# Optimization experiments

Hardware: AMD Instinct MI355X
Metric: run time of the kernel (lower is better)

## Reference

```python
import jax, jax.numpy as jnp
import numpy as np

B, S, HD, HE = 32, 2048, 1024, 1024

def setup_inputs() -> dict:
    key = jax.random.key(0)
    k1, k2, k3, k4, k5, k6 = jax.random.split(key, 6)
    decoder_hidden = jax.random.normal(k1, (B, HD), dtype=jnp.float32)
    encoder_outputs = jax.random.normal(k2, (B, S, HE), dtype=jnp.float32)
    src_mask = jax.random.randint(k3, (B, S), 0, 2) > 0
    # nn.Linear weights stored as [out, in]; apply as x @ W.T
    s_q = 1.0 / np.sqrt(HD)
    s_k = 1.0 / np.sqrt(HE)
    W_query = jax.random.uniform(k4, (HD, HD), jnp.float32, -s_q, s_q)
    W_key = jax.random.uniform(k5, (HD, HE), jnp.float32, -s_k, s_k)
    W_energy = jax.random.uniform(k6, (1, HD), jnp.float32, -s_q, s_q)
    return {
        "decoder_hidden": decoder_hidden,
        "encoder_outputs": encoder_outputs,
        "src_mask": src_mask,
        "W_query": W_query,
        "W_key": W_key,
        "W_energy": W_energy,
    }

def reference(decoder_hidden, encoder_outputs, src_mask, W_query, W_key, W_energy):
    # q: [B, 1, HD], k: [B, S, HD]
    q = (decoder_hidden @ W_query.T)[:, None, :]
    k = jnp.einsum("bse,de->bsd", encoder_outputs, W_key)
    # scores: [B, S] = v^T tanh(q + k)
    scores = jnp.einsum("bsd,d->bs", jnp.tanh(q + k), W_energy[0])
    scores = jnp.where(src_mask, scores, -1e9)
    attn_weights = jax.nn.softmax(scores, axis=-1)
    context = jnp.einsum("bs,bse->be", attn_weights, encoder_outputs)
    return context, attn_weights
```

## Files before the change

kernel.cpp:

```cpp
#include <hip/hip_runtime.h>
#include <hip/hip_bf16.h>


#define NB 32
#define SS 2048
#define HD 1024
#define HE 1024
#define MM (NB * SS)
#define NT 32

typedef float f32x4 __attribute__((ext_vector_type(4)));
typedef short bf16x8 __attribute__((ext_vector_type(8)));
typedef short short4v __attribute__((ext_vector_type(4)));

static __device__ __forceinline__ short f2bf(float f) {
    union { __hip_bfloat16 h; short s; } u;
    u.h = __float2bfloat16(f);
    return u.s;
}
static __device__ __forceinline__ float bf2f(short s) {
    union { float f; unsigned u; } u;
    u.u = ((unsigned)(unsigned short)s) << 16;
    return u.f;
}

static __device__ __forceinline__ void gload16(const void* g, const void* l) {
    __builtin_amdgcn_global_load_lds(
        (const __attribute__((address_space(1))) void*)(uintptr_t)(g),
        (__attribute__((address_space(3))) void*)(unsigned)(uintptr_t)(l),
        16, 0, 0);
}

__global__ __launch_bounds__(64) void compact_kernel(const int* __restrict__ mask,
                                                     int* __restrict__ idx,
                                                     int* __restrict__ cnt) {
    const int b = blockIdx.x;
    const int lane = threadIdx.x;
    int base = 0;
    for (int s0 = 0; s0 < SS; s0 += 64) {
        const int m = mask[b * SS + s0 + lane];
        const unsigned long long bal = __ballot(m != 0);
        const int rank = __popcll(bal & ((1ull << lane) - 1ull));
        if (m) idx[b * SS + base + rank] = s0 + lane;
        base += (int)__popcll(bal);
    }
    if (lane == 0) cnt[b] = base;
    for (int j = base + lane; j < SS; j += 64) idx[b * SS + j] = 0;
}

__global__ __launch_bounds__(256) void zero_kernel(float* __restrict__ p, int n) {
    const int i = blockIdx.x * 256 + threadIdx.x;
    if (i < n) p[i] = 0.f;
}

__global__ __launch_bounds__(256) void cvt_bf16_kernel(const float* __restrict__ in,
                                                       short* __restrict__ out, int n8) {
    int i = blockIdx.x * 256 + threadIdx.x;
    const int stride = gridDim.x * 256;
    for (; i < n8; i += stride) {
        const f32x4 a = *(const f32x4*)(in + (long)i * 8);
        const f32x4 b = *(const f32x4*)(in + (long)i * 8 + 4);
        bf16x8 o;
        o[0] = f2bf(a[0]); o[1] = f2bf(a[1]); o[2] = f2bf(a[2]); o[3] = f2bf(a[3]);
        o[4] = f2bf(b[0]); o[5] = f2bf(b[1]); o[6] = f2bf(b[2]); o[7] = f2bf(b[3]);
        *(bf16x8*)(out + (long)i * 8) = o;
    }
}

__global__ __launch_bounds__(256) void cvt_enc_kernel(const float* __restrict__ enc,
                                                      const int* __restrict__ idx,
                                                      const int* __restrict__ cnt,
                                                      short* __restrict__ encb) {
    const int b  = blockIdx.x >> 7;
    const int j0 = (blockIdx.x & 127) * 16;
    const int n  = cnt[b];
    const int nr = (n + 127) & ~127;
    if (j0 >= nr) return;
    const int j  = j0 + (threadIdx.x >> 4);
    const int c0 = (threadIdx.x & 15) * 8;
    short* dst = encb + ((long)b * SS + j) * HE + c0;
    if (j < n) {
        const float* src = enc + ((long)b * SS + idx[b * SS + j]) * HE + c0;
        #pragma unroll
        for (int u = 0; u < 8; ++u) {
            const f32x4 x = *(const f32x4*)(src + u * 128);
            const f32x4 y = *(const f32x4*)(src + u * 128 + 4);
            bf16x8 o;
            o[0] = f2bf(x[0]); o[1] = f2bf(x[1]); o[2] = f2bf(x[2]); o[3] = f2bf(x[3]);
            o[4] = f2bf(y[0]); o[5] = f2bf(y[1]); o[6] = f2bf(y[2]); o[7] = f2bf(y[3]);
            *(bf16x8*)(dst + u * 128) = o;
        }
    } else {
        const bf16x8 z = (bf16x8){0,0,0,0,0,0,0,0};
        #pragma unroll
        for (int u = 0; u < 8; ++u) *(bf16x8*)(dst + u * 128) = z;
    }
}

__global__ __launch_bounds__(256) void qproj_kernel(const float* __restrict__ dh,
                                                    const float* __restrict__ Wq,
                                                    float* __restrict__ q) {
    const int wid  = threadIdx.x >> 6;
    const int lane = threadIdx.x & 63;
    const int d    = blockIdx.x * 4 + wid;
    const float* wrow = Wq + (long)d * HD + lane * 16;
    f32x4 w0 = *(const f32x4*)(wrow + 0);
    f32x4 w1 = *(const f32x4*)(wrow + 4);
    f32x4 w2 = *(const f32x4*)(wrow + 8);
    f32x4 w3 = *(const f32x4*)(wrow + 12);
    for (int b = 0; b < NB; ++b) {
        const float* drow = dh + b * HD + lane * 16;
        f32x4 d0 = *(const f32x4*)(drow + 0);
        f32x4 d1 = *(const f32x4*)(drow + 4);
        f32x4 d2 = *(const f32x4*)(drow + 8);
        f32x4 d3 = *(const f32x4*)(drow + 12);
        f32x4 s4 = w0 * d0 + w1 * d1 + w2 * d2 + w3 * d3;
        float dot = s4[0] + s4[1] + s4[2] + s4[3];
        #pragma unroll
        for (int off = 32; off > 0; off >>= 1)
            dot += __shfl_xor(dot, off, 64);
        if (lane == 0) q[b * HD + d] = dot;
    }
}

__global__ __launch_bounds__(256, 3) void score_mfma_kernel(const short* __restrict__ encb,
                                                            const short* __restrict__ wkb,
                                                            const float* __restrict__ qv,
                                                            const float* __restrict__ ven,
                                                            const int* __restrict__ cnt,
                                                            float* __restrict__ sp) {
    __shared__ __align__(16) short As[4096];
    __shared__ __align__(16) short Bs[4096];

    const int bid   = blockIdx.x;
    const int xcd   = bid & 7;
    const int slot  = bid >> 3;
    const int mtile = xcd * 64 + (slot >> 3);
    const int nt    = slot & 7;

    const int bb   = mtile >> 4;
    const int tile = mtile & 15;
    if (tile * 128 >= cnt[bb]) return;

    const int tid  = threadIdx.x;
    const int lane = tid & 63;
    const int wid  = tid >> 6;
    const int wr   = wid >> 1;
    const int wc   = wid & 1;
    const long mbase = (long)bb * SS + tile * 128;
    const int  nbase = nt * 128;

    f32x4 acc[4][4];
    #pragma unroll
    for (int m = 0; m < 4; ++m)
        #pragma unroll
        for (int n = 0; n < 4; ++n)
            acc[m][n] = (f32x4){0.f, 0.f, 0.f, 0.f};

    const short* ag0 = encb + (mbase + (tid >> 2)) * (long)HE + (tid & 3) * 8;
    const short* ag1 = ag0 + 64 * (long)HE;
    const short* bg0 = wkb + ((long)(nbase + (tid >> 2))) * HE + (tid & 3) * 8;
    const short* bg1 = bg0 + 64 * (long)HE;

    const int frow = lane & 15;
    const int kby  = (lane >> 4) * 16;

    for (int kt = 0; kt < NT; ++kt) {
        const int ko = kt * 32;
        gload16(ag0 + ko, (char*)As + wid * 1024);
        gload16(ag1 + ko, (char*)As + 4096 + wid * 1024);
        gload16(bg0 + ko, (char*)Bs + wid * 1024);
        gload16(bg1 + ko, (char*)Bs + 4096 + wid * 1024);
        __syncthreads();

        bf16x8 af[4], bfr[4];
        #pragma unroll
        for (int m = 0; m < 4; ++m)
            af[m] = *(const bf16x8*)((const char*)As + (wr * 64 + m * 16 + frow) * 64 + kby);
        #pragma unroll
        for (int n = 0; n < 4; ++n)
            bfr[n] = *(const bf16x8*)((const char*)Bs + (wc * 64 + n * 16 + frow) * 64 + kby);
        #pragma unroll
        for (int m = 0; m < 4; ++m)
            #pragma unroll
            for (int n = 0; n < 4; ++n)
                acc[m][n] = __builtin_amdgcn_mfma_f32_16x16x32_bf16(af[m], bfr[n], acc[m][n], 0, 0, 0);
        __syncthreads();
    }

    float qq[4], vv[4];
    #pragma unroll
    for (int n = 0; n < 4; ++n) {
        const int c = nbase + wc * 64 + n * 16 + frow;
        qq[n] = qv[bb * HD + c];
        vv[n] = ven[c];
    }
    float p[4][4];
    #pragma unroll
    for (int m = 0; m < 4; ++m) {
        #pragma unroll
        for (int rg = 0; rg < 4; ++rg) {
            float s = 0.f;
            #pragma unroll
            for (int n = 0; n < 4; ++n) {
                const float x = acc[m][n][rg] + qq[n];
                const float e = __expf(2.f * x);
                const float t = 1.f - 2.f * __builtin_amdgcn_rcpf(e + 1.f);
                s += vv[n] * t;
            }
            #pragma unroll
            for (int msk = 1; msk <= 8; msk <<= 1)
                s += __shfl_xor(s, msk, 64);
            p[m][rg] = s;
        }
    }
    if ((lane & 15) == 0) {
        const int g = lane >> 4;
        float* dst = sp + (long)(nt * 2 + wc) * MM;
        #pragma unroll
        for (int m = 0; m < 4; ++m)
            #pragma unroll
            for (int rg = 0; rg < 4; ++rg)
                dst[mbase + wr * 64 + m * 16 + g * 4 + rg] = p[m][rg];
    }
}

__global__ __launch_bounds__(256) void softmax_kernel(const float* __restrict__ sp,
                                                      const int* __restrict__ idx,
                                                      const int* __restrict__ cnt,
                                                      float* __restrict__ attn,
                                                      float* __restrict__ wcomp) {
    const int b = blockIdx.x;
    const int tid = threadIdx.x;
    const int lane = tid & 63;
    const int wid = tid >> 6;
    const int n = cnt[b];
    __shared__ float red[4];
    float sc[8];
    float mx = -3.0e38f;
    #pragma unroll
    for (int i = 0; i < 8; ++i) {
        const int j = tid + i * 256;
        float v = -3.0e38f;
        if (j < n) {
            v = 0.f;
            #pragma unroll
            for (int k = 0; k < 16; ++k)
                v += sp[(long)k * MM + b * SS + j];
        }
        sc[i] = v;
        mx = fmaxf(mx, v);
    }
    #pragma unroll
    for (int off = 32; off > 0; off >>= 1)
        mx = fmaxf(mx, __shfl_xor(mx, off, 64));
    if (lane == 0) red[wid] = mx;
    __syncthreads();
    mx = fmaxf(fmaxf(red[0], red[1]), fmaxf(red[2], red[3]));
    __syncthreads();
    float sum = 0.f;
    #pragma unroll
    for (int i = 0; i < 8; ++i) {
        const float e = (sc[i] > -1.0e38f) ? __expf(sc[i] - mx) : 0.f;
        sc[i] = e;
        sum += e;
    }
    #pragma unroll
    for (int off = 32; off > 0; off >>= 1)
        sum += __shfl_xor(sum, off, 64);
    if (lane == 0) red[wid] = sum;
    __syncthreads();
    sum = red[0] + red[1] + red[2] + red[3];
    const float inv = 1.f / sum;
    #pragma unroll
    for (int i = 0; i < 8; ++i) {
        const int j = tid + i * 256;
        const float w = sc[i] * inv;
        wcomp[b * SS + j] = w;
        if (j < n) attn[b * SS + idx[b * SS + j]] = w;
    }
}

__global__ __launch_bounds__(256) void ctx_partial_kernel(const short* __restrict__ encb,
                                                          const float* __restrict__ wcomp,
                                                          const int* __restrict__ cnt,
                                                          float* __restrict__ cp) {
    const int b = blockIdx.x >> 5;
    const int chunk = blockIdx.x & 31;
    const int tid = threadIdx.x;
    float* dst = cp + ((long)(b * 32 + chunk)) * HE + tid * 4;
    if (chunk * 64 >= cnt[b]) {
        *(f32x4*)dst = (f32x4){0.f, 0.f, 0.f, 0.f};
        return;
    }
    const short* ep = encb + ((long)b * SS + chunk * 64) * HE + tid * 4;
    const float* ap = wcomp + b * SS + chunk * 64;
    f32x4 acc = (f32x4){0.f, 0.f, 0.f, 0.f};
    #pragma unroll 4
    for (int s = 0; s < 64; ++s) {
        const float w = ap[s];
        const short4v v = *(const short4v*)(ep + (long)s * HE);
        acc[0] += w * bf2f(v[0]);
        acc[1] += w * bf2f(v[1]);
        acc[2] += w * bf2f(v[2]);
        acc[3] += w * bf2f(v[3]);
    }
    *(f32x4*)dst = acc;
}

__global__ __launch_bounds__(256) void ctx_reduce_kernel(const float* __restrict__ cp,
                                                         float* __restrict__ out) {
    const int o = blockIdx.x * 256 + threadIdx.x;
    const int b = o >> 10;
    const int e = o & 1023;
    float s = 0.f;
    #pragma unroll
    for (int c = 0; c < 32; ++c)
        s += cp[((long)(b * 32 + c)) * HE + e];
    out[o] = s;
}

extern "C" void kernel_launch(void* const* d_in, const int* in_sizes, int n_in,
                              void* d_out, int out_size, void* d_ws, size_t ws_size,
                              hipStream_t stream) {
    const float* dh   = (const float*)d_in[0];
    const float* enc  = (const float*)d_in[1];
    const int*   mask = (const int*)d_in[2];
    const float* Wq   = (const float*)d_in[3];
    const float* Wk   = (const float*)d_in[4];
    const float* Ve   = (const float*)d_in[5];

    float* out  = (float*)d_out;
    float* ctx  = out;
    float* attn = out + NB * HD;

    float* ws    = (float*)d_ws;
    float* wq_   = ws;
    float* sp    = ws + 32768;
    float* cp    = sp + 16 * (long)MM;
    short* wkb   = (short*)(cp + 32 * 32 * HE);
    float* wcomp = (float*)(wkb + (long)HD * HE);
    int*   idx   = (int*)(wcomp + MM);
    int*   cnt   = idx + MM;
    short* encb  = (short*)(cnt + 64);

    compact_kernel<<<NB, 64, 0, stream>>>(mask, idx, cnt);
    zero_kernel<<<MM / 256, 256, 0, stream>>>(attn, MM);
    qproj_kernel<<<256, 256, 0, stream>>>(dh, Wq, wq_);
    cvt_bf16_kernel<<<512, 256, 0, stream>>>(Wk, wkb, HD * HE / 8);
    cvt_enc_kernel<<<NB * 128, 256, 0, stream>>>(enc, idx, cnt, encb);
    score_mfma_kernel<<<4096, 256, 0, stream>>>(encb, wkb, wq_, Ve, cnt, sp);
    softmax_kernel<<<NB, 256, 0, stream>>>(sp, idx, cnt, attn, wcomp);
    ctx_partial_kernel<<<1024, 256, 0, stream>>>(encb, wcomp, cnt, cp);
    ctx_reduce_kernel<<<128, 256, 0, stream>>>(cp, ctx);
}
```

Baseline: 187.6 us.

## Rewrite score GEMM as 256x256-tile, double-buffered, 8-phase pipelined MFMA kernel

Replaces the 128x128, single-buffered score GEMM (which syncs twice per 32-wide k-step) with 256x256 tiles on 512 threads. It uses a 128 KB double-buffered LDS with XOR swizzling and 64-wide k-steps. Global-to-LDS loads are issued in eight interleaved phases alongside the MFMA blocks, with setprio and explicit barriers, to overlap loads with compute and raise per-tile reuse. It also pads compacted rows to 256 and folds the attn zeroing into the softmax kernel, removing one launch. The risks are lower occupancy, more wasted padding rows when the per-batch mask count is small, and fragile hand-placed waitcnt/barrier sequencing.

```diff
diff --git a/kernel.cpp b/kernel.cpp
--- a/kernel.cpp
+++ b/kernel.cpp
@@ -7,7 +7,7 @@
 #define HD 1024
 #define HE 1024
 #define MM (NB * SS)
-#define NT 32
+#define NKT 16
 
 typedef float f32x4 __attribute__((ext_vector_type(4)));
 typedef short bf16x8 __attribute__((ext_vector_type(8)));
@@ -48,11 +48,6 @@
     for (int j = base + lane; j < SS; j += 64) idx[b * SS + j] = 0;
 }
 
-__global__ __launch_bounds__(256) void zero_kernel(float* __restrict__ p, int n) {
-    const int i = blockIdx.x * 256 + threadIdx.x;
-    if (i < n) p[i] = 0.f;
-}
-
 __global__ __launch_bounds__(256) void cvt_bf16_kernel(const float* __restrict__ in,
                                                        short* __restrict__ out, int n8) {
     int i = blockIdx.x * 256 + threadIdx.x;
@@ -74,7 +69,7 @@
     const int b  = blockIdx.x >> 7;
     const int j0 = (blockIdx.x & 127) * 16;
     const int n  = cnt[b];
-    const int nr = (n + 127) & ~127;
+    const int nr = (n + 255) & ~255;
     if (j0 >= nr) return;
     const int j  = j0 + (threadIdx.x >> 4);
     const int c0 = (threadIdx.x & 15) * 8;
@@ -123,70 +118,116 @@
     }
 }
 
-__global__ __launch_bounds__(256, 3) void score_mfma_kernel(const short* __restrict__ encb,
-                                                            const short* __restrict__ wkb,
-                                                            const float* __restrict__ qv,
-                                                            const float* __restrict__ ven,
-                                                            const int* __restrict__ cnt,
-                                                            float* __restrict__ sp) {
-    __shared__ __align__(16) short As[4096];
-    __shared__ __align__(16) short Bs[4096];
+__global__ __launch_bounds__(512, 2) void score_8ph_kernel(const short* __restrict__ encb,
+                                                           const short* __restrict__ wkb,
+                                                           const float* __restrict__ qv,
+                                                           const float* __restrict__ ven,
+                                                           const int* __restrict__ cnt,
+                                                           float* __restrict__ sp) {
+    __shared__ __align__(16) char Ls[131072];
 
     const int bid   = blockIdx.x;
     const int xcd   = bid & 7;
     const int slot  = bid >> 3;
-    const int mtile = xcd * 64 + (slot >> 3);
-    const int nt    = slot & 7;
-
-    const int bb   = mtile >> 4;
-    const int tile = mtile & 15;
-    if (tile * 128 >= cnt[bb]) return;
+    const int mtile = xcd * 32 + (slot >> 2);
+    const int nt    = slot & 3;
+    const int bb    = mtile >> 3;
+    const int tile  = mtile & 7;
+    if (tile * 256 >= cnt[bb]) return;
 
     const int tid  = threadIdx.x;
     const int lane = tid & 63;
     const int wid  = tid >> 6;
-    const int wr   = wid >> 1;
-    const int wc   = wid & 1;
-    const long mbase = (long)bb * SS + tile * 128;
-    const int  nbase = nt * 128;
-
-    f32x4 acc[4][4];
-    #pragma unroll
-    for (int m = 0; m < 4; ++m)
-        #pragma unroll
-        for (int n = 0; n < 4; ++n)
-            acc[m][n] = (f32x4){0.f, 0.f, 0.f, 0.f};
-
-    const short* ag0 = encb + (mbase + (tid >> 2)) * (long)HE + (tid & 3) * 8;
-    const short* ag1 = ag0 + 64 * (long)HE;
-    const short* bg0 = wkb + ((long)(nbase + (tid >> 2))) * HE + (tid & 3) * 8;
-    const short* bg1 = bg0 + 64 * (long)HE;
+    const int wr   = wid >> 2;
+    const int wc   = wid & 3;
+    const long mbase = (long)bb * SS + tile * 256;
+    const int  nbase = nt * 256;
+
+    f32x4 acc[8][4] = {};
+    bf16x8 bfr[2][4];
+
+    const int srow  = tid >> 3;
+    const int swoff = ((tid & 7) ^ (srow & 7)) * 8;
+    const short* aG = encb + (mbase + srow) * (long)HE + swoff;
+    const short* bG = wkb + ((long)(nbase + srow)) * HE + swoff;
+
+    #define STG(OPG, OPBASE, BUF, HALF, KT)                                          \
+        do {                                                                         \
+            gload16(OPG + (KT) * 64 + (HALF) * 128 * (long)HE,                       \
+                    Ls + (OPBASE) + (BUF) * 32768 + (HALF) * 16384 + (wid * 64) * 16); \
+            gload16(OPG + (KT) * 64 + (HALF) * 128 * (long)HE + 64 * (long)HE,       \
+                    Ls + (OPBASE) + (BUF) * 32768 + (HALF) * 16384 + 8192 + (wid * 64) * 16); \
+        } while (0)
 
     const int frow = lane & 15;
-    const int kby  = (lane >> 4) * 16;
-
-    for (int kt = 0; kt < NT; ++kt) {
-        const int ko = kt * 32;
-        gload16(ag0 + ko, (char*)As + wid * 1024);
-        gload16(ag1 + ko, (char*)As + 4096 + wid * 1024);
-        gload16(bg0 + ko, (char*)Bs + wid * 1024);
-        gload16(bg1 + ko, (char*)Bs + 4096 + wid * 1024);
-        __syncthreads();
-
-        bf16x8 af[4], bfr[4];
-        #pragma unroll
-        for (int m = 0; m < 4; ++m)
-            af[m] = *(const bf16x8*)((const char*)As + (wr * 64 + m * 16 + frow) * 64 + kby);
-        #pragma unroll
-        for (int n = 0; n < 4; ++n)
-            bfr[n] = *(const bf16x8*)((const char*)Bs + (wc * 64 + n * 16 + frow) * 64 + kby);
-        #pragma unroll
-        for (int m = 0; m < 4; ++m)
-            #pragma unroll
-            for (int n = 0; n < 4; ++n)
-                acc[m][n] = __builtin_amdgcn_mfma_f32_16x16x32_bf16(af[m], bfr[n], acc[m][n], 0, 0, 0);
-        __syncthreads();
-    }
+    const int kb0  = (((lane >> 4) ^ (frow & 7)) * 16);
+    const int kb1  = kb0 ^ 64;
+    const char* aRd = Ls + wr * 16384 + frow * 128;
+    int bOff[4];
+    #pragma unroll
+    for (int n = 0; n < 4; ++n) {
+        const int RB = wc * 64 + n * 16 + frow;
+        bOff[n] = 65536 + (RB >> 7) * 16384 + (RB & 127) * 128;
+    }
+
+    #define PH(BUF, Q, FIRST, STAGE_CODE, CLOSE_CODE)                                \
+        do {                                                                         \
+            if (FIRST) {                                                             \
+                _Pragma("unroll")                                                    \
+                for (int n = 0; n < 4; ++n) {                                        \
+                    bfr[0][n] = *(const bf16x8*)(Ls + bOff[n] + (BUF) * 32768 + kb0);\
+                    bfr[1][n] = *(const bf16x8*)(Ls + bOff[n] + (BUF) * 32768 + kb1);\
+                }                                                                    \
+            }                                                                        \
+            bf16x8 a0k0 = *(const bf16x8*)(aRd + (BUF) * 32768 + (2 * (Q)) * 2048 + kb0);     \
+            bf16x8 a0k1 = *(const bf16x8*)(aRd + (BUF) * 32768 + (2 * (Q)) * 2048 + kb1);     \
+            bf16x8 a1k0 = *(const bf16x8*)(aRd + (BUF) * 32768 + (2 * (Q) + 1) * 2048 + kb0); \
+            bf16x8 a1k1 = *(const bf16x8*)(aRd + (BUF) * 32768 + (2 * (Q) + 1) * 2048 + kb1); \
+            STAGE_CODE;                                                              \
+            asm volatile("s_barrier" ::: "memory");                                  \
+            asm volatile("s_waitcnt lgkmcnt(0)" ::: "memory");                       \
+            __builtin_amdgcn_sched_barrier(0);                                       \
+            __builtin_amdgcn_s_setprio(1);                                           \
+            _Pragma("unroll")                                                        \
+            for (int n = 0; n < 4; ++n) {                                            \
+                acc[2*(Q)][n]   = __builtin_amdgcn_mfma_f32_16x16x32_bf16(a0k0, bfr[0][n], acc[2*(Q)][n], 0, 0, 0);   \
+                acc[2*(Q)+1][n] = __builtin_amdgcn_mfma_f32_16x16x32_bf16(a1k0, bfr[0][n], acc[2*(Q)+1][n], 0, 0, 0); \
+                acc[2*(Q)][n]   = __builtin_amdgcn_mfma_f32_16x16x32_bf16(a0k1, bfr[1][n], acc[2*(Q)][n], 0, 0, 0);   \
+                acc[2*(Q)+1][n] = __builtin_amdgcn_mfma_f32_16x16x32_bf16(a1k1, bfr[1][n], acc[2*(Q)+1][n], 0, 0, 0); \
+            }                                                                        \
+            __builtin_amdgcn_s_setprio(0);                                           \
+            __builtin_amdgcn_sched_barrier(0);                                       \
+            CLOSE_CODE;                                                              \
+        } while (0)
+
+    STG(bG, 65536, 0, 0, 0);  STG(bG, 65536, 0, 1, 0);
+    STG(aG, 0,     0, 0, 0);  STG(aG, 0,     0, 1, 0);
+    STG(bG, 65536, 1, 0, 1);  STG(bG, 65536, 1, 1, 1);
+    asm volatile("s_waitcnt vmcnt(4)\ns_barrier" ::: "memory");
+
+    for (int t = 0; t < 8; ++t) {
+        const int k0 = 2 * t;
+        PH(0, 0, true,  { STG(aG, 0, 1, 0, k0 + 1); },
+           asm volatile("s_barrier" ::: "memory"));
+        PH(0, 1, false, { STG(aG, 0, 1, 1, k0 + 1); },
+           asm volatile("s_barrier" ::: "memory"));
+        PH(0, 2, false, { if (t < 7) STG(bG, 65536, 0, 0, k0 + 2); },
+           asm volatile("s_barrier" ::: "memory"));
+        PH(0, 3, false, { if (t < 7) STG(bG, 65536, 0, 1, k0 + 2); },
+           { if (t < 7) asm volatile("s_waitcnt vmcnt(4)\ns_barrier" ::: "memory");
+             else       asm volatile("s_waitcnt vmcnt(0)\ns_barrier" ::: "memory"); });
+        PH(1, 0, true,  { if (t < 7) STG(aG, 0, 0, 0, k0 + 2); },
+           asm volatile("s_barrier" ::: "memory"));
+        PH(1, 1, false, { if (t < 7) STG(aG, 0, 0, 1, k0 + 2); },
+           asm volatile("s_barrier" ::: "memory"));
+        PH(1, 2, false, { if (t < 7) STG(bG, 65536, 1, 0, k0 + 3); },
+           asm volatile("s_barrier" ::: "memory"));
+        PH(1, 3, false, { if (t < 7) STG(bG, 65536, 1, 1, k0 + 3); },
+           { if (t < 7) asm volatile("s_waitcnt vmcnt(4)\ns_barrier" ::: "memory");
+             else       asm volatile("s_barrier" ::: "memory"); });
+    }
+    #undef PH
+    #undef STG
 
     float qq[4], vv[4];
     #pragma unroll
@@ -195,9 +236,9 @@
         qq[n] = qv[bb * HD + c];
         vv[n] = ven[c];
     }
-    float p[4][4];
-    #pragma unroll
-    for (int m = 0; m < 4; ++m) {
+    float p[8][4];
+    #pragma unroll
+    for (int m = 0; m < 8; ++m) {
         #pragma unroll
         for (int rg = 0; rg < 4; ++rg) {
             float s = 0.f;
@@ -216,12 +257,12 @@
     }
     if ((lane & 15) == 0) {
         const int g = lane >> 4;
-        float* dst = sp + (long)(nt * 2 + wc) * MM;
-        #pragma unroll
-        for (int m = 0; m < 4; ++m)
+        float* dst = sp + (long)(nt * 4 + wc) * MM;
+        #pragma unroll
+        for (int m = 0; m < 8; ++m)
             #pragma unroll
             for (int rg = 0; rg < 4; ++rg)
-                dst[mbase + wr * 64 + m * 16 + g * 4 + rg] = p[m][rg];
+                dst[mbase + wr * 128 + m * 16 + g * 4 + rg] = p[m][rg];
     }
 }
 
@@ -235,6 +276,9 @@
     const int lane = tid & 63;
     const int wid = tid >> 6;
     const int n = cnt[b];
+    #pragma unroll
+    for (int i = 0; i < 8; ++i)
+        attn[b * SS + tid + i * 256] = 0.f;
     __shared__ float red[4];
     float sc[8];
     float mx = -3.0e38f;
@@ -345,11 +389,10 @@
     short* encb  = (short*)(cnt + 64);
 
     compact_kernel<<<NB, 64, 0, stream>>>(mask, idx, cnt);
-    zero_kernel<<<MM / 256, 256, 0, stream>>>(attn, MM);
     qproj_kernel<<<256, 256, 0, stream>>>(dh, Wq, wq_);
     cvt_bf16_kernel<<<512, 256, 0, stream>>>(Wk, wkb, HD * HE / 8);
     cvt_enc_kernel<<<NB * 128, 256, 0, stream>>>(enc, idx, cnt, encb);
-    score_mfma_kernel<<<4096, 256, 0, stream>>>(encb, wkb, wq_, Ve, cnt, sp);
+    score_8ph_kernel<<<1024, 512, 0, stream>>>(encb, wkb, wq_, Ve, cnt, sp);
     softmax_kernel<<<NB, 256, 0, stream>>>(sp, idx, cnt, attn, wcomp);
     ctx_partial_kernel<<<1024, 256, 0, stream>>>(encb, wcomp, cnt, cp);
     ctx_reduce_kernel<<<128, 256, 0, stream>>>(cp, ctx);
```

Result: slower. 191.6 us (+2.1%).
